# Kernel tuning notes

Measured on AMD Instinct MI355X. Metric: run time of the kernel, lower is better.

The kernel has to match this reference:

```python
import jax, jax.numpy as jnp
import numpy as np

B, N, F, K, O = 4, 4096, 32, 6, 128


def setup_inputs() -> dict:
    key = jax.random.key(0)
    k1, k2, k3, k4 = jax.random.split(key, 4)
    x = jax.random.normal(k1, (B, N, F), dtype=jnp.float32)
    # dense per-batch (normalized-Laplacian-like) operator; scaled for stable recurrence
    L = jax.random.normal(k2, (B, N, N), dtype=jnp.float32) / np.float32(np.sqrt(N))
    # per-order projection weights lins[k]: in -> out  (stored [K, F, O])
    W = jax.random.normal(k3, (K, F, O), dtype=jnp.float32) * 0.1
    # per-order scalar 1x1 'theta' weights lins_theta[k]
    theta = jax.random.normal(k4, (K,), dtype=jnp.float32) * 0.1
    return {"x": x, "L": L, "W": W, "theta": theta}


def reference(x, L, W, theta):
    # Chebyshev recurrence: T0 = x, T1 = L@x, T_k = 2 L@T_{k-1} - T_{k-2}
    # Each order: elementwise scalar theta_k (the 1x1 Linear) then Linear(F->O), summed.
    k_orders = W.shape[0]
    x0 = x                                                   # [B,N,F]
    out = theta[0] * jnp.einsum('bnf,fo->bno', x0, W[0])     # [B,N,O]
    if k_orders > 1:
        x1 = jnp.matmul(L, x0)                               # [B,N,F]
        out = out + theta[1] * jnp.einsum('bnf,fo->bno', x1, W[1])
    for k in range(2, k_orders):
        x2 = 2.0 * jnp.matmul(L, x1) - x0
        out = out + theta[k] * jnp.einsum('bnf,fo->bno', x2, W[k])
        x0, x1 = x1, x2
    return out
```

## Files before the change

### kernel.cpp

```cpp
#include <hip/hip_runtime.h>

#define N4 4096
#define FF 32
#define KK 6
#define OO 128
#define BB 4

typedef __attribute__((ext_vector_type(8))) short  short8;
typedef __attribute__((ext_vector_type(4))) float  f32x4;
typedef __attribute__((ext_vector_type(4))) int    i32x4;
typedef __attribute__((ext_vector_type(2))) unsigned int u32x2;

__device__ __forceinline__ float b2f(unsigned short h) {
    union { float f; unsigned u; } v; v.u = ((unsigned)h) << 16; return v.f;
}
__device__ __forceinline__ unsigned short f2b(float f) {
    union { float f; unsigned u; } v; v.f = f;
    unsigned r = (v.u + 0x7FFFu + ((v.u >> 16) & 1u)) >> 16;
    return (unsigned short)r;
}

__global__ __launch_bounds__(256) void make_wc(const float* __restrict__ W,
                                               const float* __restrict__ theta,
                                               unsigned short* __restrict__ Wc) {
    int idx = blockIdx.x * 256 + threadIdx.x;
    int k = idx >> 12;
    Wc[idx] = f2b(theta[k] * W[idx]);
}

__global__ __launch_bounds__(256) void x_to_t(const float* __restrict__ x,
                                              unsigned short* __restrict__ T0) {
    __shared__ __align__(16) unsigned short Ol[32][72];
    int tid = threadIdx.x, bid = blockIdx.x;
    int b = bid >> 6; long n0 = (long)(bid & 63) * 64;
    int nl = tid >> 2, fg = (tid & 3) * 8;
    const float* src = x + ((long)b * N4 + n0 + nl) * FF + fg;
    f32x4 v0 = *(const f32x4*)src;
    f32x4 v1 = *(const f32x4*)(src + 4);
#pragma unroll
    for (int e = 0; e < 4; ++e) {
        Ol[fg + e][nl]     = f2b(v0[e]);
        Ol[fg + 4 + e][nl] = f2b(v1[e]);
    }
    __syncthreads();
    int f = tid >> 3, col = (tid & 7) * 8;
    *(i32x4*)(T0 + ((long)b * FF + f) * N4 + n0 + col) = *(const i32x4*)&Ol[f][col];
}

template <int MODE>
__global__ __launch_bounds__(256) void gemm_pass(const float* __restrict__ Lf,
                                                 const unsigned short* __restrict__ Lb,
                                                 unsigned short* __restrict__ LbOut,
                                                 const unsigned short* __restrict__ Tt,
                                                 float* __restrict__ P) {
    __shared__ __align__(16) unsigned short Al[128][72];
    __shared__ __align__(16) unsigned short Bl[32][72];
    int tid = threadIdx.x, bid = blockIdx.x;
    int s = bid & 3, mb = (bid >> 2) & 31, b = bid >> 7;
    long m0 = (long)mb * 128;
    long k0 = (long)s * 1024;
    int wave = tid >> 6, lane = tid & 63, quad = lane >> 4, l16 = lane & 15;

    f32x4 acc00 = {0.f,0.f,0.f,0.f}, acc01 = {0.f,0.f,0.f,0.f};
    f32x4 acc10 = {0.f,0.f,0.f,0.f}, acc11 = {0.f,0.f,0.f,0.f};

    for (int kc = 0; kc < 1024; kc += 64) {
        if (MODE != 1) {
            const float* src = Lf + (long)b * N4 * N4;
#pragma unroll
            for (int it = 0; it < 8; ++it) {
                int row = it * 16 + (tid >> 4);
                int col = (tid & 15) * 4;
                long g = (m0 + row) * (long)N4 + k0 + kc + col;
                f32x4 v = *(const f32x4*)(src + g);
                u32x2 pk;
                pk[0] = (unsigned)f2b(v[0]) | ((unsigned)f2b(v[1]) << 16);
                pk[1] = (unsigned)f2b(v[2]) | ((unsigned)f2b(v[3]) << 16);
                *(u32x2*)&Al[row][col] = pk;
                if (MODE == 0)
                    *(u32x2*)(LbOut + (long)b * N4 * N4 + g) = pk;
            }
        } else {
            const unsigned short* src = Lb + (long)b * N4 * N4;
#pragma unroll
            for (int it = 0; it < 4; ++it) {
                int row = it * 32 + (tid >> 3);
                int col = (tid & 7) * 8;
                long g = (m0 + row) * (long)N4 + k0 + kc + col;
                *(i32x4*)&Al[row][col] = *(const i32x4*)(src + g);
            }
        }
        {
            int f = tid >> 3, col = (tid & 7) * 8;
            *(i32x4*)&Bl[f][col] =
                *(const i32x4*)(Tt + ((long)b * FF + f) * N4 + k0 + kc + col);
        }
        __syncthreads();
#pragma unroll
        for (int kk = 0; kk < 64; kk += 32) {
            short8 a0 = *(const short8*)&Al[wave * 32 + l16][kk + quad * 8];
            short8 a1 = *(const short8*)&Al[wave * 32 + 16 + l16][kk + quad * 8];
            short8 b0 = *(const short8*)&Bl[l16][kk + quad * 8];
            short8 b1 = *(const short8*)&Bl[16 + l16][kk + quad * 8];
            acc00 = __builtin_amdgcn_mfma_f32_16x16x32_bf16(a0, b0, acc00, 0, 0, 0);
            acc01 = __builtin_amdgcn_mfma_f32_16x16x32_bf16(a0, b1, acc01, 0, 0, 0);
            acc10 = __builtin_amdgcn_mfma_f32_16x16x32_bf16(a1, b0, acc10, 0, 0, 0);
            acc11 = __builtin_amdgcn_mfma_f32_16x16x32_bf16(a1, b1, acc11, 0, 0, 0);
        }
        __syncthreads();
    }
    float* Pp = P + (((long)s * BB + b) * N4 + m0) * FF;
#pragma unroll
    for (int r = 0; r < 4; ++r) {
        int row0 = wave * 32 + quad * 4 + r;
        int row1 = row0 + 16;
        Pp[(long)row0 * FF + l16]      = acc00[r];
        Pp[(long)row0 * FF + 16 + l16] = acc01[r];
        Pp[(long)row1 * FF + l16]      = acc10[r];
        Pp[(long)row1 * FF + 16 + l16] = acc11[r];
    }
}

__global__ __launch_bounds__(256) void reduce_pass(const float* __restrict__ P,
                                                   const unsigned short* __restrict__ Tpp,
                                                   unsigned short* __restrict__ Tout,
                                                   float a, float c) {
    __shared__ __align__(16) unsigned short Tpl[32][72];
    __shared__ __align__(16) unsigned short Ol[32][72];
    int tid = threadIdx.x, bid = blockIdx.x;
    int b = bid >> 6; long n0 = (long)(bid & 63) * 64;
    if (Tpp) {
        int f = tid >> 3, col = (tid & 7) * 8;
        *(i32x4*)&Tpl[f][col] = *(const i32x4*)(Tpp + ((long)b * FF + f) * N4 + n0 + col);
    }
    __syncthreads();
    int nl = tid >> 2, fg = (tid & 3) * 8;
    const float* p0 = P + ((long)b * N4 + n0 + nl) * FF + fg;
    float sum[8];
#pragma unroll
    for (int e = 0; e < 8; ++e) sum[e] = 0.f;
#pragma unroll
    for (int s = 0; s < 4; ++s) {
        const float* ps = p0 + (long)s * BB * N4 * FF;
        f32x4 v0 = *(const f32x4*)ps;
        f32x4 v1 = *(const f32x4*)(ps + 4);
#pragma unroll
        for (int e = 0; e < 4; ++e) { sum[e] += v0[e]; sum[4 + e] += v1[e]; }
    }
#pragma unroll
    for (int e = 0; e < 8; ++e) {
        float val = a * sum[e];
        if (Tpp) val += c * b2f(Tpl[fg + e][nl]);
        Ol[fg + e][nl] = f2b(val);
    }
    __syncthreads();
    int f = tid >> 3, col = (tid & 7) * 8;
    *(i32x4*)(Tout + ((long)b * FF + f) * N4 + n0 + col) = *(const i32x4*)&Ol[f][col];
}

__global__ __launch_bounds__(256) void proj(const unsigned short* __restrict__ T,
                                            const unsigned short* __restrict__ Wc,
                                            float* __restrict__ out) {
    __shared__ __align__(16) unsigned short Tl[192][72];
    __shared__ __align__(16) unsigned short Wl[192][64];
    int tid = threadIdx.x, bid = blockIdx.x;
    int b = bid >> 7; int rem = bid & 127;
    long n0 = (long)(rem >> 1) * 64; int oh = rem & 1;
#pragma unroll
    for (int it = 0; it < 6; ++it) {
        int row = it * 32 + (tid >> 3);
        int col = (tid & 7) * 8;
        int k = row >> 5, f = row & 31;
        *(i32x4*)&Tl[row][col] =
            *(const i32x4*)(T + (((long)k * BB + b) * FF + f) * N4 + n0 + col);
        *(i32x4*)&Wl[row][col] = *(const i32x4*)(Wc + (long)row * OO + oh * 64 + col);
    }
    __syncthreads();
    int ol = tid & 63;
    int nb = (tid >> 6) * 16;
    float acc[16];
#pragma unroll
    for (int r = 0; r < 16; ++r) acc[r] = 0.f;
    for (int kf = 0; kf < 192; ++kf) {
        float w = b2f(Wl[kf][ol]);
#pragma unroll
        for (int rv = 0; rv < 2; ++rv) {
            short8 tv = *(const short8*)&Tl[kf][nb + rv * 8];
#pragma unroll
            for (int e = 0; e < 8; ++e)
                acc[rv * 8 + e] += b2f((unsigned short)tv[e]) * w;
        }
    }
    int o = oh * 64 + ol;
#pragma unroll
    for (int r = 0; r < 16; ++r)
        out[((long)b * N4 + n0 + nb + r) * OO + o] = acc[r];
}

extern "C" void kernel_launch(void* const* d_in, const int* in_sizes, int n_in,
                              void* d_out, int out_size, void* d_ws, size_t ws_size,
                              hipStream_t stream) {
    const float* x     = (const float*)d_in[0];
    const float* L     = (const float*)d_in[1];
    const float* W     = (const float*)d_in[2];
    const float* theta = (const float*)d_in[3];
    float* out = (float*)d_out;
    char* ws = (char*)d_ws;

    const size_t LB_BYTES = (size_t)BB * N4 * N4 * 2;
    const size_t T_SLOT   = (size_t)BB * FF * N4;
    const size_t T_BYTES  = (size_t)KK * T_SLOT * 2;
    const size_t P_BYTES  = (size_t)4 * BB * N4 * FF * 4;
    const size_t WC_BYTES = (size_t)KK * FF * OO * 2;

    bool haveL = ws_size >= LB_BYTES + T_BYTES + P_BYTES + WC_BYTES;
    size_t off = haveL ? LB_BYTES : 0;
    unsigned short* Lb = (unsigned short*)ws;
    unsigned short* T  = (unsigned short*)(ws + off);
    float*          P  = (float*)(ws + off + T_BYTES);
    unsigned short* Wc = (unsigned short*)(ws + off + T_BYTES + P_BYTES);

    make_wc<<<96, 256, 0, stream>>>(W, theta, Wc);
    x_to_t<<<256, 256, 0, stream>>>(x, T);

    if (haveL)
        gemm_pass<0><<<512, 256, 0, stream>>>(L, nullptr, Lb, T, P);
    else
        gemm_pass<2><<<512, 256, 0, stream>>>(L, nullptr, nullptr, T, P);
    reduce_pass<<<256, 256, 0, stream>>>(P, nullptr, T + 1 * T_SLOT, 1.f, 0.f);

    for (int k = 2; k < KK; ++k) {
        if (haveL)
            gemm_pass<1><<<512, 256, 0, stream>>>(nullptr, Lb, nullptr, T + (k - 1) * T_SLOT, P);
        else
            gemm_pass<2><<<512, 256, 0, stream>>>(L, nullptr, nullptr, T + (k - 1) * T_SLOT, P);
        reduce_pass<<<256, 256, 0, stream>>>(P, T + (k - 2) * T_SLOT, T + k * T_SLOT, 2.f, -1.f);
    }

    proj<<<512, 256, 0, stream>>>(T, Wc, out);
}
```

Baseline: 561.7 us.

## Replace LDS-tiled L@T GEMM with register-streaming MFMA and separate bf16 transcode

Replaces the shared-memory tiled GEMM with a kernel that loads A and B fragments straight from global memory into registers, using a 4-deep software prefetch ring and no barriers. Each wave now owns a 16-row strip instead of 32 rows, and the grid grows to 1024 blocks. The fused fp32-to-bf16 conversion of L in the first pass moves into a separate transcode kernel. The aim is to stream L at bandwidth without LDS staging or syncs. The cost is an extra full pass over L for transcoding, and the T operand is reloaded by every wave with less reuse.

```diff
diff --git a/kernel.cpp b/kernel.cpp
--- a/kernel.cpp
+++ b/kernel.cpp
@@ -47,77 +47,82 @@
     *(i32x4*)(T0 + ((long)b * FF + f) * N4 + n0 + col) = *(const i32x4*)&Ol[f][col];
 }
 
-template <int MODE>
-__global__ __launch_bounds__(256) void gemm_pass(const float* __restrict__ Lf,
-                                                 const unsigned short* __restrict__ Lb,
-                                                 unsigned short* __restrict__ LbOut,
-                                                 const unsigned short* __restrict__ Tt,
-                                                 float* __restrict__ P) {
-    __shared__ __align__(16) unsigned short Al[128][72];
-    __shared__ __align__(16) unsigned short Bl[32][72];
-    int tid = threadIdx.x, bid = blockIdx.x;
-    int s = bid & 3, mb = (bid >> 2) & 31, b = bid >> 7;
-    long m0 = (long)mb * 128;
+__global__ __launch_bounds__(256) void transcode(const float* __restrict__ L,
+                                                 unsigned short* __restrict__ Lb) {
+    long g = (long)blockIdx.x * 256 + threadIdx.x;
+    long base = g * 8;
+    f32x4 v0 = *(const f32x4*)(L + base);
+    f32x4 v1 = *(const f32x4*)(L + base + 4);
+    i32x4 pk;
+    pk[0] = (unsigned)f2b(v0[0]) | ((unsigned)f2b(v0[1]) << 16);
+    pk[1] = (unsigned)f2b(v0[2]) | ((unsigned)f2b(v0[3]) << 16);
+    pk[2] = (unsigned)f2b(v1[0]) | ((unsigned)f2b(v1[1]) << 16);
+    pk[3] = (unsigned)f2b(v1[2]) | ((unsigned)f2b(v1[3]) << 16);
+    *(i32x4*)(Lb + base) = pk;
+}
+
+template <bool AF32>
+__global__ __launch_bounds__(256) void gemm_stream(const unsigned short* __restrict__ Ab,
+                                                   const float* __restrict__ Af,
+                                                   const unsigned short* __restrict__ Tt,
+                                                   float* __restrict__ P) {
+    int tid = threadIdx.x, bid = blockIdx.x;
+    int s = bid & 3, b = (bid >> 2) & 3, sg = bid >> 4;
+    int wave = tid >> 6, lane = tid & 63, quad = lane >> 4, l16 = lane & 15;
+    long m0 = (long)(sg * 4 + wave) * 16;
     long k0 = (long)s * 1024;
-    int wave = tid >> 6, lane = tid & 63, quad = lane >> 4, l16 = lane & 15;
-
-    f32x4 acc00 = {0.f,0.f,0.f,0.f}, acc01 = {0.f,0.f,0.f,0.f};
-    f32x4 acc10 = {0.f,0.f,0.f,0.f}, acc11 = {0.f,0.f,0.f,0.f};
-
-    for (int kc = 0; kc < 1024; kc += 64) {
-        if (MODE != 1) {
-            const float* src = Lf + (long)b * N4 * N4;
-#pragma unroll
-            for (int it = 0; it < 8; ++it) {
-                int row = it * 16 + (tid >> 4);
-                int col = (tid & 15) * 4;
-                long g = (m0 + row) * (long)N4 + k0 + kc + col;
-                f32x4 v = *(const f32x4*)(src + g);
-                u32x2 pk;
-                pk[0] = (unsigned)f2b(v[0]) | ((unsigned)f2b(v[1]) << 16);
-                pk[1] = (unsigned)f2b(v[2]) | ((unsigned)f2b(v[3]) << 16);
-                *(u32x2*)&Al[row][col] = pk;
-                if (MODE == 0)
-                    *(u32x2*)(LbOut + (long)b * N4 * N4 + g) = pk;
+
+    const unsigned short* Ap = AF32 ? nullptr
+        : Ab + ((long)b * N4 + m0 + l16) * N4 + k0 + quad * 8;
+    const float* Fp = AF32
+        ? Af + ((long)b * N4 + m0 + l16) * N4 + k0 + quad * 8 : nullptr;
+    const unsigned short* B0p = Tt + ((long)b * FF + l16) * N4 + k0 + quad * 8;
+    const unsigned short* B1p = B0p + (long)16 * N4;
+
+    f32x4 acc0 = {0.f,0.f,0.f,0.f}, acc1 = {0.f,0.f,0.f,0.f};
+
+    auto ldA = [&](int ks) -> short8 {
+        if (AF32) {
+            f32x4 v0 = *(const f32x4*)(Fp + ks * 32);
+            f32x4 v1 = *(const f32x4*)(Fp + ks * 32 + 4);
+            short8 r;
+#pragma unroll
+            for (int e = 0; e < 4; ++e) {
+                r[e]     = (short)f2b(v0[e]);
+                r[4 + e] = (short)f2b(v1[e]);
             }
-        } else {
-            const unsigned short* src = Lb + (long)b * N4 * N4;
-#pragma unroll
-            for (int it = 0; it < 4; ++it) {
-                int row = it * 32 + (tid >> 3);
-                int col = (tid & 7) * 8;
-                long g = (m0 + row) * (long)N4 + k0 + kc + col;
-                *(i32x4*)&Al[row][col] = *(const i32x4*)(src + g);
-            }
+            return r;
         }
-        {
-            int f = tid >> 3, col = (tid & 7) * 8;
-            *(i32x4*)&Bl[f][col] =
-                *(const i32x4*)(Tt + ((long)b * FF + f) * N4 + k0 + kc + col);
+        return *(const short8*)(Ap + ks * 32);
+    };
+    auto ldB = [&](const unsigned short* p, int ks) -> short8 {
+        return *(const short8*)(p + ks * 32);
+    };
+
+    short8 Ar[4], B0r[4], B1r[4];
+#pragma unroll
+    for (int i = 0; i < 4; ++i) {
+        Ar[i] = ldA(i); B0r[i] = ldB(B0p, i); B1r[i] = ldB(B1p, i);
+    }
+#pragma unroll 4
+    for (int ks = 0; ks < 32; ++ks) {
+        int sl = ks & 3;
+        short8 a = Ar[sl], b0 = B0r[sl], b1 = B1r[sl];
+        if (ks + 4 < 32) {
+            Ar[sl]  = ldA(ks + 4);
+            B0r[sl] = ldB(B0p, ks + 4);
+            B1r[sl] = ldB(B1p, ks + 4);
         }
-        __syncthreads();
-#pragma unroll
-        for (int kk = 0; kk < 64; kk += 32) {
-            short8 a0 = *(const short8*)&Al[wave * 32 + l16][kk + quad * 8];
-            short8 a1 = *(const short8*)&Al[wave * 32 + 16 + l16][kk + quad * 8];
-            short8 b0 = *(const short8*)&Bl[l16][kk + quad * 8];
-            short8 b1 = *(const short8*)&Bl[16 + l16][kk + quad * 8];
-            acc00 = __builtin_amdgcn_mfma_f32_16x16x32_bf16(a0, b0, acc00, 0, 0, 0);
-            acc01 = __builtin_amdgcn_mfma_f32_16x16x32_bf16(a0, b1, acc01, 0, 0, 0);
-            acc10 = __builtin_amdgcn_mfma_f32_16x16x32_bf16(a1, b0, acc10, 0, 0, 0);
-            acc11 = __builtin_amdgcn_mfma_f32_16x16x32_bf16(a1, b1, acc11, 0, 0, 0);
-        }
-        __syncthreads();
-    }
+        acc0 = __builtin_amdgcn_mfma_f32_16x16x32_bf16(a, b0, acc0, 0, 0, 0);
+        acc1 = __builtin_amdgcn_mfma_f32_16x16x32_bf16(a, b1, acc1, 0, 0, 0);
+    }
+
     float* Pp = P + (((long)s * BB + b) * N4 + m0) * FF;
 #pragma unroll
     for (int r = 0; r < 4; ++r) {
-        int row0 = wave * 32 + quad * 4 + r;
-        int row1 = row0 + 16;
-        Pp[(long)row0 * FF + l16]      = acc00[r];
-        Pp[(long)row0 * FF + 16 + l16] = acc01[r];
-        Pp[(long)row1 * FF + l16]      = acc10[r];
-        Pp[(long)row1 * FF + 16 + l16] = acc11[r];
+        int row = quad * 4 + r;
+        Pp[(long)row * FF + l16]      = acc0[r];
+        Pp[(long)row * FF + 16 + l16] = acc1[r];
     }
 }
 
@@ -224,16 +229,19 @@
     x_to_t<<<256, 256, 0, stream>>>(x, T);
 
     if (haveL)
-        gemm_pass<0><<<512, 256, 0, stream>>>(L, nullptr, Lb, T, P);
+        transcode<<<32768, 256, 0, stream>>>(L, Lb);
+
+    if (haveL)
+        gemm_stream<false><<<1024, 256, 0, stream>>>(Lb, nullptr, T, P);
     else
-        gemm_pass<2><<<512, 256, 0, stream>>>(L, nullptr, nullptr, T, P);
+        gemm_stream<true><<<1024, 256, 0, stream>>>(nullptr, L, T, P);
     reduce_pass<<<256, 256, 0, stream>>>(P, nullptr, T + 1 * T_SLOT, 1.f, 0.f);
 
     for (int k = 2; k < KK; ++k) {
         if (haveL)
-            gemm_pass<1><<<512, 256, 0, stream>>>(nullptr, Lb, nullptr, T + (k - 1) * T_SLOT, P);
+            gemm_stream<false><<<1024, 256, 0, stream>>>(Lb, nullptr, T + (k - 1) * T_SLOT, P);
         else
-            gemm_pass<2><<<512, 256, 0, stream>>>(L, nullptr, nullptr, T + (k - 1) * T_SLOT, P);
+            gemm_stream<true><<<1024, 256, 0, stream>>>(nullptr, L, T + (k - 1) * T_SLOT, P);
         reduce_pass<<<256, 256, 0, stream>>>(P, T + (k - 2) * T_SLOT, T + k * T_SLOT, 2.f, -1.f);
     }
 
```

Result: slower. 650.5 us (+15.8%).
